# Optimization experiments

Measured on AMD Instinct MI355X. Metric: run time of the kernel, lower is better.

## Reference

```python
import jax, jax.numpy as jnp
import numpy as np

B, N, D = 256, 2048, 128
ANCHOR = 0


def setup_inputs() -> dict:
    key = jax.random.key(0)
    k0, k1, k2, k3 = jax.random.split(key, 4)
    return {
        "embs": jax.random.normal(k0, (B * N, D), jnp.float32),
        "W1": jax.random.normal(k1, (D, 2 * D), jnp.float32) / np.sqrt(2 * D),
        "b1": jnp.zeros((D,), jnp.float32),
        "W2": jax.random.normal(k2, (D, D), jnp.float32) / np.sqrt(D),
        "b2": jnp.zeros((D,), jnp.float32),
        "batch_idx": jax.random.randint(k3, (B * N,), 0, B, dtype=jnp.int32),
        "batch_size": B,
        "num_nodes": N,
        "num_anchors": ANCHOR,
    }


def reference(embs, W1, b1, W2, b2, batch_idx, batch_size, num_nodes, num_anchors):
    # static boolean mask over nodes (num_anchors is a Python int)
    non_target = np.arange(num_nodes) != num_anchors
    e = embs.reshape(batch_size, num_nodes, -1)            # (B, N, D)
    non_targets = e[:, non_target]                          # (B, N-1, D)
    target = e[:, ~non_target]                              # (B, 1, D)
    x = jnp.concatenate(
        (jnp.broadcast_to(target, non_targets.shape), non_targets), axis=-1
    )                                                       # (B, N-1, 2D)
    h = jax.nn.relu(jnp.einsum("bnk,dk->bnd", x, W1) + b1)  # (B, N-1, D)
    y = jnp.einsum("bnk,dk->bnd", h, W2) + b2               # (B, N-1, D)
    y = y.reshape(batch_size * (num_nodes - 1), -1)
    bidx = batch_idx.reshape(batch_size, num_nodes)[:, non_target].reshape(-1)
    return jax.ops.segment_sum(y, bidx, num_segments=batch_size)  # (B, D)
```

## Files before the change

kernel.cpp:

```cpp
#include <hip/hip_runtime.h>

#define B_SZ    256
#define N_NODES 2048
#define D_DIM   128
#define NROW_TOT (B_SZ * N_NODES)

typedef __attribute__((ext_vector_type(8))) short short8;
typedef __attribute__((ext_vector_type(4))) float f32x4;

#define WS_W1BF   0
#define WS_COUNT  65536
#define WS_ACC    66560
#define WS_P      197632
#define CAP       4096
#define WS_NEEDED (WS_P + B_SZ * CAP * 4)

__device__ __forceinline__ unsigned pk2(float x, float y) {
    unsigned a = __float_as_uint(x), b = __float_as_uint(y);
    a += 0x7fffu + ((a >> 16) & 1u);
    b += 0x7fffu + ((b >> 16) & 1u);
    return (a >> 16) | (b & 0xffff0000u);
}

__global__ void k_prep(const float* __restrict__ W1, unsigned* __restrict__ w1bf,
                       const int* __restrict__ bidx, int* __restrict__ count,
                       int* __restrict__ P) {
    if (blockIdx.x < 64) {
        int i = blockIdx.x * 256 + threadIdx.x;
        float2 f = ((const float2*)W1)[i];
        w1bf[i] = pk2(f.x, f.y);
        return;
    }
    __shared__ int lh[256];
    __shared__ int sbase[256];
    int blk = blockIdx.x - 64;
    int t = threadIdx.x;
    lh[t] = 0;
    __syncthreads();
    int base = blk * 1024 + t * 4;
    int4 v = ((const int4*)bidx)[blk * 256 + t];
    int p0 = -1, p1 = -1, p2 = -1, p3 = -1;
    if (((base + 0) & 2047) != 0) p0 = atomicAdd(&lh[v.x], 1);
    if (((base + 1) & 2047) != 0) p1 = atomicAdd(&lh[v.y], 1);
    if (((base + 2) & 2047) != 0) p2 = atomicAdd(&lh[v.z], 1);
    if (((base + 3) & 2047) != 0) p3 = atomicAdd(&lh[v.w], 1);
    __syncthreads();
    if (lh[t]) sbase[t] = atomicAdd(&count[t], lh[t]);
    __syncthreads();
    if (p0 >= 0) P[v.x * CAP + sbase[v.x] + p0] = base + 0;
    if (p1 >= 0) P[v.y * CAP + sbase[v.y] + p1] = base + 1;
    if (p2 >= 0) P[v.z * CAP + sbase[v.z] + p2] = base + 2;
    if (p3 >= 0) P[v.w * CAP + sbase[v.w] + p3] = base + 3;
}

#define CHUNK   64
#define ESTRIDE 272

__global__ __launch_bounds__(1024) void k_main(
    const float* __restrict__ embs, const float* __restrict__ b1,
    const short* __restrict__ w1bf, const int* __restrict__ P,
    const int* __restrict__ count, float* __restrict__ ACC)
{
    __shared__ char  tgt[256 * 256];
    __shared__ char  estage[2][CHUNK * ESTRIDE];
    __shared__ float segacc[D_DIM];

    int tid = threadIdx.x;
    int s   = blockIdx.x;
    int cnt = count[s];
    const int pbase = s * CAP;

    if (tid < D_DIM) segacc[tid] = 0.f;

#pragma unroll
    for (int it = 0; it < 4; it++) {
        int task = it * 1024 + tid;
        int tr = task >> 4;
        int p  = task & 15;
        const float4* src = (const float4*)(embs + ((size_t)(tr << 11)) * D_DIM) + p * 2;
        float4 g0 = src[0], g1 = src[1];
        uint4 w = make_uint4(pk2(g0.x, g0.y), pk2(g0.z, g0.w),
                             pk2(g1.x, g1.y), pk2(g1.z, g1.w));
        *(uint4*)(tgt + ((tr * 256 + p * 16) ^ ((tr & 7) << 4))) = w;
    }

    int lane = tid & 63;
    int wid  = tid >> 6;
    int rt   = wid & 3;
    int cg   = wid >> 2;
    int q    = lane >> 4;
    int i15  = lane & 15;

    short8 bfrag[8][2];
#pragma unroll
    for (int kt = 0; kt < 8; kt++)
#pragma unroll
        for (int ct = 0; ct < 2; ct++) {
            int n = cg * 32 + ct * 16 + i15;
            bfrag[kt][ct] = *(const short8*)(w1bf + n * 256 + kt * 32 + q * 8);
        }
    float b1c0 = b1[cg * 32 + i15];
    float b1c1 = b1[cg * 32 + 16 + i15];
    float asum0 = 0.f, asum1 = 0.f;

    int srow = tid >> 3;
    int part = tid & 7;
    bool stager = tid < 512;

    int nchunk = (cnt + CHUNK - 1) >> 6;

    float4 f0, f1, f2, f3;
    int bcur = 0, ridx_next = 0;

    if (nchunk > 0 && stager) {
        int gr = pbase + (srow < cnt ? srow : cnt - 1);
        int r0 = P[gr];
        bcur = r0 >> 11;
        const float4* src = (const float4*)(embs + (size_t)r0 * D_DIM) + part * 4;
        f0 = src[0]; f1 = src[1]; f2 = src[2]; f3 = src[3];
        if (nchunk > 1) {
            int rl = CHUNK + srow;
            ridx_next = P[pbase + (rl < cnt ? rl : cnt - 1)];
        }
    }
    __syncthreads();

    for (int c = 0; c < nchunk; c++) {
        char* wb = estage[c & 1];
        if (stager) {
            uint4 wa = make_uint4(pk2(f0.x, f0.y), pk2(f0.z, f0.w),
                                  pk2(f1.x, f1.y), pk2(f1.z, f1.w));
            uint4 wbv = make_uint4(pk2(f2.x, f2.y), pk2(f2.z, f2.w),
                                   pk2(f3.x, f3.y), pk2(f3.z, f3.w));
            uint4* dst = (uint4*)(wb + srow * ESTRIDE + part * 32);
            dst[0] = wa; dst[1] = wbv;
            if (part == 0) *(int*)(wb + srow * ESTRIDE + 256) = bcur;
        }
        __syncthreads();

        if (stager && c + 1 < nchunk) {
            int r = ridx_next;
            bcur = r >> 11;
            const float4* src = (const float4*)(embs + (size_t)r * D_DIM) + part * 4;
            f0 = src[0]; f1 = src[1]; f2 = src[2]; f3 = src[3];
            if (c + 2 < nchunk) {
                int rl = (c + 2) * CHUNK + srow;
                ridx_next = P[pbase + (rl < cnt ? rl : cnt - 1)];
            }
        }

        f32x4 m0 = {0.f, 0.f, 0.f, 0.f}, m1 = {0.f, 0.f, 0.f, 0.f};
        int row = rt * 16 + i15;
        int b = *(const int*)(wb + row * ESTRIDE + 256);
        unsigned sw = ((unsigned)(b & 7)) << 4;
        unsigned tb = ((unsigned)b << 8) + (unsigned)(q * 16);
#pragma unroll
        for (int kt = 0; kt < 4; kt++) {
            short8 a = *(const short8*)(tgt + ((tb + kt * 64) ^ sw));
            m0 = __builtin_amdgcn_mfma_f32_16x16x32_bf16(a, bfrag[kt][0], m0, 0, 0, 0);
            m1 = __builtin_amdgcn_mfma_f32_16x16x32_bf16(a, bfrag[kt][1], m1, 0, 0, 0);
        }
        const char* ar = wb + row * ESTRIDE + q * 16;
#pragma unroll
        for (int kt = 0; kt < 4; kt++) {
            short8 a = *(const short8*)(ar + kt * 64);
            m0 = __builtin_amdgcn_mfma_f32_16x16x32_bf16(a, bfrag[kt + 4][0], m0, 0, 0, 0);
            m1 = __builtin_amdgcn_mfma_f32_16x16x32_bf16(a, bfrag[kt + 4][1], m1, 0, 0, 0);
        }
        int rbase = c * 64 + rt * 16 + q * 4;
#pragma unroll
        for (int j = 0; j < 4; j++) {
            if (rbase + j < cnt) {
                asum0 += fmaxf(m0[j] + b1c0, 0.f);
                asum1 += fmaxf(m1[j] + b1c1, 0.f);
            }
        }
    }

    asum0 += __shfl_xor(asum0, 16, 64);
    asum0 += __shfl_xor(asum0, 32, 64);
    asum1 += __shfl_xor(asum1, 16, 64);
    asum1 += __shfl_xor(asum1, 32, 64);
    if (lane < 16) {
        atomicAdd(&segacc[cg * 32 + lane],      asum0);
        atomicAdd(&segacc[cg * 32 + 16 + lane], asum1);
    }
    __syncthreads();
    if (tid < D_DIM) ACC[s * D_DIM + tid] = segacc[tid];
}

__global__ void k_out(const float* __restrict__ ACC, const float* __restrict__ W2,
                      const float* __restrict__ b2, const int* __restrict__ count,
                      float* __restrict__ out) {
    __shared__ float a[D_DIM];
    int s = blockIdx.x, d = threadIdx.x;
    a[d] = ACC[s * D_DIM + d];
    __syncthreads();
    float sum = (float)count[s] * b2[d];
    const float4* w = (const float4*)(W2 + d * D_DIM);
#pragma unroll
    for (int k = 0; k < 32; k++) {
        float4 wv = w[k];
        sum += a[4 * k + 0] * wv.x + a[4 * k + 1] * wv.y
             + a[4 * k + 2] * wv.z + a[4 * k + 3] * wv.w;
    }
    out[s * D_DIM + d] = sum;
}

extern "C" void kernel_launch(void* const* d_in, const int* in_sizes, int n_in,
                              void* d_out, int out_size, void* d_ws, size_t ws_size,
                              hipStream_t stream) {
    const float* embs = (const float*)d_in[0];
    const float* W1   = (const float*)d_in[1];
    const float* b1   = (const float*)d_in[2];
    const float* W2   = (const float*)d_in[3];
    const float* b2   = (const float*)d_in[4];
    const int*   bidx = (const int*)d_in[5];

    char* ws = (char*)d_ws;
    unsigned* w1bf_u = (unsigned*)(ws + WS_W1BF);
    short*    w1bf   = (short*)(ws + WS_W1BF);
    int*   count  = (int*)(ws + WS_COUNT);
    float* ACC    = (float*)(ws + WS_ACC);
    int*   P      = (int*)(ws + WS_P);

    hipMemsetAsync(count, 0, 256 * sizeof(int), stream);
    k_prep<<<576, 256, 0, stream>>>(W1, w1bf_u, bidx, count, P);
    k_main<<<256, 1024, 0, stream>>>(embs, b1, w1bf, P, count, ACC);
    k_out<<<256, 128, 0, stream>>>(ACC, W2, b2, count, (float*)d_out);
}
```

Measured before the change: 408.3 us.

## Precompute target-half of first layer per batch and split segments across two blocks

```diff
diff --git a/kernel.cpp b/kernel.cpp
--- a/kernel.cpp
+++ b/kernel.cpp
@@ -10,8 +10,9 @@
 
 #define WS_W1BF   0
 #define WS_COUNT  65536
-#define WS_ACC    66560
-#define WS_P      197632
+#define WS_T      66560
+#define WS_ACC    197632
+#define WS_P      459776
 #define CAP       4096
 #define WS_NEEDED (WS_P + B_SZ * CAP * 4)
 
@@ -24,17 +25,36 @@
 
 __global__ void k_prep(const float* __restrict__ W1, unsigned* __restrict__ w1bf,
                        const int* __restrict__ bidx, int* __restrict__ count,
-                       int* __restrict__ P) {
+                       int* __restrict__ P, const float* __restrict__ embs,
+                       const float* __restrict__ b1, float* __restrict__ T) {
+    int t = threadIdx.x;
     if (blockIdx.x < 64) {
-        int i = blockIdx.x * 256 + threadIdx.x;
+        int i = blockIdx.x * 256 + t;
         float2 f = ((const float2*)W1)[i];
         w1bf[i] = pk2(f.x, f.y);
         return;
     }
+    if (blockIdx.x >= 576) {
+        int tb = blockIdx.x - 576;
+        __shared__ float trow[128];
+        if (t < 128) trow[t] = embs[(size_t)(tb << 11) * D_DIM + t];
+        __syncthreads();
+        if (t < 128) {
+            const float4* w = (const float4*)(W1 + t * 256);
+            float s = 0.f;
+#pragma unroll
+            for (int k = 0; k < 32; k++) {
+                float4 wv = w[k];
+                s += trow[4 * k + 0] * wv.x + trow[4 * k + 1] * wv.y
+                   + trow[4 * k + 2] * wv.z + trow[4 * k + 3] * wv.w;
+            }
+            T[tb * 128 + t] = s + b1[t];
+        }
+        return;
+    }
     __shared__ int lh[256];
     __shared__ int sbase[256];
     int blk = blockIdx.x - 64;
-    int t = threadIdx.x;
     lh[t] = 0;
     __syncthreads();
     int base = blk * 1024 + t * 4;
@@ -56,123 +76,123 @@
 #define CHUNK   64
 #define ESTRIDE 272
 
-__global__ __launch_bounds__(1024) void k_main(
-    const float* __restrict__ embs, const float* __restrict__ b1,
+__global__ __launch_bounds__(512, 4) void k_main(
+    const float* __restrict__ embs, const float* __restrict__ Tm,
     const short* __restrict__ w1bf, const int* __restrict__ P,
     const int* __restrict__ count, float* __restrict__ ACC)
 {
-    __shared__ char  tgt[256 * 256];
-    __shared__ char  estage[2][CHUNK * ESTRIDE];
+    __shared__ __align__(16) char estage[2][CHUNK * ESTRIDE];
+    __shared__ int   bidarr[2][64];
     __shared__ float segacc[D_DIM];
 
-    int tid = threadIdx.x;
-    int s   = blockIdx.x;
-    int cnt = count[s];
+    int tid  = threadIdx.x;
+    int g    = blockIdx.x;
+    int s    = g >> 1;
+    int half = g & 1;
+    int cnt  = count[s];
     const int pbase = s * CAP;
 
     if (tid < D_DIM) segacc[tid] = 0.f;
-
-#pragma unroll
-    for (int it = 0; it < 4; it++) {
-        int task = it * 1024 + tid;
-        int tr = task >> 4;
-        int p  = task & 15;
-        const float4* src = (const float4*)(embs + ((size_t)(tr << 11)) * D_DIM) + p * 2;
-        float4 g0 = src[0], g1 = src[1];
-        uint4 w = make_uint4(pk2(g0.x, g0.y), pk2(g0.z, g0.w),
-                             pk2(g1.x, g1.y), pk2(g1.z, g1.w));
-        *(uint4*)(tgt + ((tr * 256 + p * 16) ^ ((tr & 7) << 4))) = w;
-    }
 
     int lane = tid & 63;
     int wid  = tid >> 6;
-    int rt   = wid & 3;
-    int cg   = wid >> 2;
+    int rt   = wid & 1;
+    int cg   = wid >> 1;
     int q    = lane >> 4;
     int i15  = lane & 15;
 
-    short8 bfrag[8][2];
-#pragma unroll
-    for (int kt = 0; kt < 8; kt++)
+    short8 bfrag[4][2];
+#pragma unroll
+    for (int kt = 0; kt < 4; kt++)
 #pragma unroll
         for (int ct = 0; ct < 2; ct++) {
             int n = cg * 32 + ct * 16 + i15;
-            bfrag[kt][ct] = *(const short8*)(w1bf + n * 256 + kt * 32 + q * 8);
-        }
-    float b1c0 = b1[cg * 32 + i15];
-    float b1c1 = b1[cg * 32 + 16 + i15];
-    float asum0 = 0.f, asum1 = 0.f;
+            bfrag[kt][ct] = *(const short8*)(w1bf + n * 256 + 128 + kt * 32 + q * 8);
+        }
 
     int srow = tid >> 3;
     int part = tid & 7;
-    bool stager = tid < 512;
-
-    int nchunk = (cnt + CHUNK - 1) >> 6;
+
+    int nct = (cnt + CHUNK - 1) >> 6;
+    int myn = (nct > half) ? ((nct - half + 1) >> 1) : 0;
 
     float4 f0, f1, f2, f3;
     int bcur = 0, ridx_next = 0;
 
-    if (nchunk > 0 && stager) {
-        int gr = pbase + (srow < cnt ? srow : cnt - 1);
-        int r0 = P[gr];
+    if (myn > 0) {
+        int rl = half * 64 + srow;
+        int r0 = P[pbase + (rl < cnt ? rl : cnt - 1)];
         bcur = r0 >> 11;
         const float4* src = (const float4*)(embs + (size_t)r0 * D_DIM) + part * 4;
         f0 = src[0]; f1 = src[1]; f2 = src[2]; f3 = src[3];
-        if (nchunk > 1) {
-            int rl = CHUNK + srow;
-            ridx_next = P[pbase + (rl < cnt ? rl : cnt - 1)];
-        }
-    }
-    __syncthreads();
-
-    for (int c = 0; c < nchunk; c++) {
-        char* wb = estage[c & 1];
-        if (stager) {
+        if (myn > 1) {
+            int rl2 = (half + 2) * 64 + srow;
+            ridx_next = P[pbase + (rl2 < cnt ? rl2 : cnt - 1)];
+        }
+    }
+    __syncthreads();
+
+    float asum0 = 0.f, asum1 = 0.f;
+
+    for (int i = 0; i < myn; i++) {
+        int c = half + 2 * i;
+        char* wb = estage[i & 1];
+        {
             uint4 wa = make_uint4(pk2(f0.x, f0.y), pk2(f0.z, f0.w),
                                   pk2(f1.x, f1.y), pk2(f1.z, f1.w));
-            uint4 wbv = make_uint4(pk2(f2.x, f2.y), pk2(f2.z, f2.w),
-                                   pk2(f3.x, f3.y), pk2(f3.z, f3.w));
+            uint4 wv = make_uint4(pk2(f2.x, f2.y), pk2(f2.z, f2.w),
+                                  pk2(f3.x, f3.y), pk2(f3.z, f3.w));
             uint4* dst = (uint4*)(wb + srow * ESTRIDE + part * 32);
-            dst[0] = wa; dst[1] = wbv;
-            if (part == 0) *(int*)(wb + srow * ESTRIDE + 256) = bcur;
+            dst[0] = wa; dst[1] = wv;
+            if (part == 0) bidarr[i & 1][srow] = bcur;
         }
         __syncthreads();
 
-        if (stager && c + 1 < nchunk) {
+        int4 bh0 = *(const int4*)&bidarr[i & 1][rt * 32 + q * 4];
+        int4 bh1 = *(const int4*)&bidarr[i & 1][rt * 32 + 16 + q * 4];
+        int c0 = cg * 32 + i15;
+        float tv0[4][2], tv1[4][2];
+#pragma unroll
+        for (int j = 0; j < 4; j++) {
+            int b0 = (&bh0.x)[j], b1i = (&bh1.x)[j];
+            tv0[j][0] = Tm[b0 * 128 + c0];  tv0[j][1] = Tm[b0 * 128 + c0 + 16];
+            tv1[j][0] = Tm[b1i * 128 + c0]; tv1[j][1] = Tm[b1i * 128 + c0 + 16];
+        }
+
+        if (i + 1 < myn) {
             int r = ridx_next;
             bcur = r >> 11;
             const float4* src = (const float4*)(embs + (size_t)r * D_DIM) + part * 4;
             f0 = src[0]; f1 = src[1]; f2 = src[2]; f3 = src[3];
-            if (c + 2 < nchunk) {
-                int rl = (c + 2) * CHUNK + srow;
+            if (i + 2 < myn) {
+                int rl = (c + 4) * 64 + srow;
                 ridx_next = P[pbase + (rl < cnt ? rl : cnt - 1)];
             }
         }
 
-        f32x4 m0 = {0.f, 0.f, 0.f, 0.f}, m1 = {0.f, 0.f, 0.f, 0.f};
-        int row = rt * 16 + i15;
-        int b = *(const int*)(wb + row * ESTRIDE + 256);
-        unsigned sw = ((unsigned)(b & 7)) << 4;
-        unsigned tb = ((unsigned)b << 8) + (unsigned)(q * 16);
+        f32x4 m00 = {0,0,0,0}, m01 = {0,0,0,0}, m10 = {0,0,0,0}, m11 = {0,0,0,0};
+        const char* ar0 = wb + (rt * 32 + i15) * ESTRIDE + q * 16;
+        const char* ar1 = ar0 + 16 * ESTRIDE;
 #pragma unroll
         for (int kt = 0; kt < 4; kt++) {
-            short8 a = *(const short8*)(tgt + ((tb + kt * 64) ^ sw));
-            m0 = __builtin_amdgcn_mfma_f32_16x16x32_bf16(a, bfrag[kt][0], m0, 0, 0, 0);
-            m1 = __builtin_amdgcn_mfma_f32_16x16x32_bf16(a, bfrag[kt][1], m1, 0, 0, 0);
-        }
-        const char* ar = wb + row * ESTRIDE + q * 16;
-#pragma unroll
-        for (int kt = 0; kt < 4; kt++) {
-            short8 a = *(const short8*)(ar + kt * 64);
-            m0 = __builtin_amdgcn_mfma_f32_16x16x32_bf16(a, bfrag[kt + 4][0], m0, 0, 0, 0);
-            m1 = __builtin_amdgcn_mfma_f32_16x16x32_bf16(a, bfrag[kt + 4][1], m1, 0, 0, 0);
-        }
-        int rbase = c * 64 + rt * 16 + q * 4;
+            short8 a0 = *(const short8*)(ar0 + kt * 64);
+            short8 a1 = *(const short8*)(ar1 + kt * 64);
+            m00 = __builtin_amdgcn_mfma_f32_16x16x32_bf16(a0, bfrag[kt][0], m00, 0, 0, 0);
+            m01 = __builtin_amdgcn_mfma_f32_16x16x32_bf16(a0, bfrag[kt][1], m01, 0, 0, 0);
+            m10 = __builtin_amdgcn_mfma_f32_16x16x32_bf16(a1, bfrag[kt][0], m10, 0, 0, 0);
+            m11 = __builtin_amdgcn_mfma_f32_16x16x32_bf16(a1, bfrag[kt][1], m11, 0, 0, 0);
+        }
+        int rb0 = c * 64 + rt * 32 + q * 4;
+        int rb1 = rb0 + 16;
 #pragma unroll
         for (int j = 0; j < 4; j++) {
-            if (rbase + j < cnt) {
-                asum0 += fmaxf(m0[j] + b1c0, 0.f);
-                asum1 += fmaxf(m1[j] + b1c1, 0.f);
+            if (rb0 + j < cnt) {
+                asum0 += fmaxf(m00[j] + tv0[j][0], 0.f);
+                asum1 += fmaxf(m01[j] + tv0[j][1], 0.f);
+            }
+            if (rb1 + j < cnt) {
+                asum0 += fmaxf(m10[j] + tv1[j][0], 0.f);
+                asum1 += fmaxf(m11[j] + tv1[j][1], 0.f);
             }
         }
     }
@@ -186,7 +206,7 @@
         atomicAdd(&segacc[cg * 32 + 16 + lane], asum1);
     }
     __syncthreads();
-    if (tid < D_DIM) ACC[s * D_DIM + tid] = segacc[tid];
+    if (tid < D_DIM) ACC[g * D_DIM + tid] = segacc[tid];
 }
 
 __global__ void k_out(const float* __restrict__ ACC, const float* __restrict__ W2,
@@ -194,7 +214,7 @@
                       float* __restrict__ out) {
     __shared__ float a[D_DIM];
     int s = blockIdx.x, d = threadIdx.x;
-    a[d] = ACC[s * D_DIM + d];
+    a[d] = ACC[(2 * s) * D_DIM + d] + ACC[(2 * s + 1) * D_DIM + d];
     __syncthreads();
     float sum = (float)count[s] * b2[d];
     const float4* w = (const float4*)(W2 + d * D_DIM);
@@ -221,11 +241,12 @@
     unsigned* w1bf_u = (unsigned*)(ws + WS_W1BF);
     short*    w1bf   = (short*)(ws + WS_W1BF);
     int*   count  = (int*)(ws + WS_COUNT);
+    float* T      = (float*)(ws + WS_T);
     float* ACC    = (float*)(ws + WS_ACC);
     int*   P      = (int*)(ws + WS_P);
 
     hipMemsetAsync(count, 0, 256 * sizeof(int), stream);
-    k_prep<<<576, 256, 0, stream>>>(W1, w1bf_u, bidx, count, P);
-    k_main<<<256, 1024, 0, stream>>>(embs, b1, w1bf, P, count, ACC);
+    k_prep<<<832, 256, 0, stream>>>(W1, w1bf_u, bidx, count, P, embs, b1, T);
+    k_main<<<512, 512, 0, stream>>>(embs, T, w1bf, P, count, ACC);
     k_out<<<256, 128, 0, stream>>>(ACC, W2, b2, count, (float*)d_out);
 }
```

Measured after the change: 403.4 us. About the same (-1.2%).
